# Optimization experiments

Measured on AMD Instinct MI355X. Metric: run time of the kernel, lower is better.

The kernel has to match this reference:

```python
import jax, jax.numpy as jnp
import numpy as np

ATTENTION_DIM = 256
MAX_STATE_SIZE = 2000
LOCATION_FILTER = 32
LOCATION_KERNEL = 31
TEMPERATURE = 1.0
CUMULATIVE = True
MASK_VAL = -2.0 ** 32 + 1


def setup_inputs() -> dict:
    key = jax.random.key(0)
    ks = jax.random.split(key, 8)
    B, T, A, F, K = 64, 2000, ATTENTION_DIM, LOCATION_FILTER, LOCATION_KERNEL
    query = jax.random.normal(ks[0], (B, A), dtype=jnp.float32)
    prev_weights = jax.random.uniform(ks[1], (B, MAX_STATE_SIZE), dtype=jnp.float32)
    w_memory = jax.random.normal(ks[2], (B, T, A), dtype=jnp.float32)
    memory_lengths = jax.random.randint(ks[3], (B,), 1, T + 1, dtype=jnp.int32)
    conv_w = jax.random.normal(ks[4], (K, 1, F), dtype=jnp.float32) * 0.1
    conv_b = jnp.zeros((F,), dtype=jnp.float32)
    loc_w = jax.random.normal(ks[5], (F, A), dtype=jnp.float32) * 0.1
    score_v = jax.random.normal(ks[6], (A,), dtype=jnp.float32)
    score_b = jnp.zeros((A,), dtype=jnp.float32)
    return {
        "query": query,
        "prev_weights": prev_weights,
        "w_memory": w_memory,
        "memory_lengths": memory_lengths,
        "conv_w": conv_w,
        "conv_b": conv_b,
        "loc_w": loc_w,
        "score_v": score_v,
        "score_b": score_b,
    }


def reference(query, prev_weights, w_memory, memory_lengths, conv_w, conv_b, loc_w, score_v, score_b):
    B, T, A = w_memory.shape
    # location features: conv over previous alignments [B, T, 1] -> [B, T, F]
    align_prev = prev_weights[:, :T][..., None]
    f = jax.lax.conv_general_dilated(
        align_prev, conv_w, window_strides=(1,), padding="SAME",
        dimension_numbers=("NWC", "WIO", "NWC")) + conv_b
    processed_loc = jnp.einsum("btf,fa->bta", f, loc_w)  # [B, T, A]
    # Bahdanau additive score -> [B, T]
    energy = jnp.einsum(
        "a,bta->bt", score_v,
        jnp.tanh(w_memory + query[:, None, :] + processed_loc + score_b)) / TEMPERATURE
    mask = jnp.arange(T)[None, :] < memory_lengths[:, None]
    energy = jnp.where(mask, energy, MASK_VAL)
    alignments = jax.nn.softmax(energy, axis=1)
    # pad to max_state_size (static pad amount)
    output = jnp.pad(alignments, ((0, 0), (0, MAX_STATE_SIZE - T)))
    new_weights = output + prev_weights if CUMULATIVE else output
    return output, new_weights
```

## Files before the change

### kernel.cpp

```cpp
#include <hip/hip_runtime.h>
#include <cstddef>

#define B_  64
#define T_  2000
#define A_  256
#define K_  31
#define F_  32
#define TT_ 128

__device__ __forceinline__ float fast_tanh(float x) {
  float p = __expf(x + x);
  float r = __builtin_amdgcn_rcpf(p + 1.0f);
  return fmaf(-2.0f, r, 1.0f);
}

__device__ __forceinline__ float4 ld4(const float* p) {
  return *(const float4*)p;
}

__device__ __forceinline__ float rfl(float x) {
  return __int_as_float(__builtin_amdgcn_readfirstlane(__float_as_int(x)));
}

__global__ __launch_bounds__(256) void prep_kernel(
    const float* __restrict__ conv_w, const float* __restrict__ conv_b,
    const float* __restrict__ loc_w, const float* __restrict__ query,
    const float* __restrict__ score_b, float* __restrict__ W2,
    float* __restrict__ qb) {
  const int a = threadIdx.x;
  const int blk = blockIdx.x;
  if (blk < K_) {
    float acc = 0.f;
    #pragma unroll
    for (int f = 0; f < F_; ++f) acc = fmaf(conv_w[blk * F_ + f], loc_w[f * A_ + a], acc);
    W2[blk * A_ + a] = acc;
  } else {
    const int b = blk - K_;
    float acc = 0.f;
    #pragma unroll
    for (int f = 0; f < F_; ++f) acc = fmaf(conv_b[f], loc_w[f * A_ + a], acc);
    qb[b * A_ + a] = query[b * A_ + a] + score_b[a] + acc;
  }
}

__global__ __attribute__((amdgpu_flat_work_group_size(256, 256),
                          amdgpu_waves_per_eu(2, 4)))
void energy_kernel(
    const float* __restrict__ wmem, const float* __restrict__ pw,
    const float* __restrict__ qb, const float* __restrict__ W2,
    const float* __restrict__ score_v, float* __restrict__ energy) {
  const int b = blockIdx.y;
  const int t0 = blockIdx.x * TT_;
  const int tid = threadIdx.x;
  const int lane = tid & 63;
  const int wv = tid >> 6;

  __shared__ __align__(16) float lds_W2[K_ * A_];
  __shared__ __align__(16) float lds_pw[TT_ + 36];

  for (int idx = tid * 4; idx < K_ * A_; idx += 256 * 4)
    *(float4*)&lds_W2[idx] = ld4(W2 + idx);

  if (tid < TT_ + 36) {
    const int g = t0 - 15 + tid;
    lds_pw[tid] = (g >= 0 && g < T_) ? pw[b * T_ + g] : 0.f;
  }
  __syncthreads();

  const float4 qb4 = ld4(qb + b * A_ + 4 * lane);
  const float4 v4  = ld4(score_v + 4 * lane);
  const float* wrow = wmem + (size_t)b * T_ * A_ + 4 * lane;
  const float* w2l  = lds_W2 + 4 * lane;

  const int rbase = 32 * wv;

  #pragma unroll 1
  for (int i = 0; i < 8; ++i) {
    const int widx = rbase + 4 * i;

    float4 w4[4];
    #pragma unroll
    for (int j = 0; j < 4; ++j) {
      const int t = t0 + widx + j;
      const int tc = t < T_ ? t : T_ - 1;
      w4[j] = ld4(wrow + (size_t)tc * A_);
    }

    float s[36];
    #pragma unroll
    for (int m = 0; m < 9; ++m) {
      const float4 t4 = ld4(&lds_pw[widx + 4 * m]);
      s[4 * m + 0] = rfl(t4.x); s[4 * m + 1] = rfl(t4.y);
      s[4 * m + 2] = rfl(t4.z); s[4 * m + 3] = rfl(t4.w);
    }

    float4 pl[4];
    #pragma unroll
    for (int j = 0; j < 4; ++j) pl[j] = make_float4(0.f, 0.f, 0.f, 0.f);
    #pragma unroll
    for (int k = 0; k < K_; ++k) {
      const float4 w2k = ld4(w2l + k * A_);
      #pragma unroll
      for (int j = 0; j < 4; ++j) {
        pl[j].x = fmaf(s[j + k], w2k.x, pl[j].x);
        pl[j].y = fmaf(s[j + k], w2k.y, pl[j].y);
        pl[j].z = fmaf(s[j + k], w2k.z, pl[j].z);
        pl[j].w = fmaf(s[j + k], w2k.w, pl[j].w);
      }
    }

    #pragma unroll
    for (int j = 0; j < 4; ++j) {
      const int t = t0 + widx + j;
      const float tx = fast_tanh(w4[j].x + qb4.x + pl[j].x);
      const float ty = fast_tanh(w4[j].y + qb4.y + pl[j].y);
      const float tz = fast_tanh(w4[j].z + qb4.z + pl[j].z);
      const float tw = fast_tanh(w4[j].w + qb4.w + pl[j].w);
      float e = fmaf(v4.x, tx, fmaf(v4.y, ty, fmaf(v4.z, tz, v4.w * tw)));
      #pragma unroll
      for (int m = 1; m < 64; m <<= 1) e += __shfl_xor(e, m, 64);
      if (lane == 0 && t < T_) energy[b * T_ + t] = e;
    }
  }
}

__global__ __launch_bounds__(256) void softmax_kernel(
    const float* __restrict__ energy, const float* __restrict__ pw,
    const int* __restrict__ lens, float* __restrict__ out) {
  const int b = blockIdx.x;
  const int tid = threadIdx.x;
  const int len = lens[b];
  __shared__ float red[4];
  const float L2E = 1.4426950408889634f;

  float mx = -3.4e38f;
  for (int t = tid; t < T_; t += 256)
    if (t < len) mx = fmaxf(mx, energy[b * T_ + t]);
  #pragma unroll
  for (int m = 1; m < 64; m <<= 1) mx = fmaxf(mx, __shfl_xor(mx, m, 64));
  if ((tid & 63) == 0) red[tid >> 6] = mx;
  __syncthreads();
  mx = fmaxf(fmaxf(red[0], red[1]), fmaxf(red[2], red[3]));
  __syncthreads();

  float sm = 0.f;
  for (int t = tid; t < T_; t += 256)
    if (t < len) sm += __builtin_amdgcn_exp2f((energy[b * T_ + t] - mx) * L2E);
  #pragma unroll
  for (int m = 1; m < 64; m <<= 1) sm += __shfl_xor(sm, m, 64);
  if ((tid & 63) == 0) red[tid >> 6] = sm;
  __syncthreads();
  sm = red[0] + red[1] + red[2] + red[3];
  const float inv = 1.0f / sm;

  for (int t = tid; t < T_; t += 256) {
    float o = 0.f;
    if (t < len)
      o = __builtin_amdgcn_exp2f((energy[b * T_ + t] - mx) * L2E) * inv;
    out[b * T_ + t] = o;
    out[B_ * T_ + b * T_ + t] = o + pw[b * T_ + t];
  }
}

extern "C" void kernel_launch(void* const* d_in, const int* in_sizes, int n_in,
                              void* d_out, int out_size, void* d_ws, size_t ws_size,
                              hipStream_t stream) {
  const float* query  = (const float*)d_in[0];
  const float* prev   = (const float*)d_in[1];
  const float* wmem   = (const float*)d_in[2];
  const int*   lens   = (const int*)d_in[3];
  const float* conv_w = (const float*)d_in[4];
  const float* conv_b = (const float*)d_in[5];
  const float* loc_w  = (const float*)d_in[6];
  const float* sv     = (const float*)d_in[7];
  const float* sb     = (const float*)d_in[8];
  float* out = (float*)d_out;
  float* ws  = (float*)d_ws;

  float* W2     = ws;
  float* qb     = ws + K_ * A_;
  float* energy = ws + K_ * A_ + B_ * A_;

  prep_kernel<<<K_ + B_, 256, 0, stream>>>(conv_w, conv_b, loc_w, query, sb, W2, qb);

  dim3 grid((T_ + TT_ - 1) / TT_, B_);
  energy_kernel<<<grid, 256, 0, stream>>>(wmem, prev, qb, W2, sv, energy);

  softmax_kernel<<<B_, 256, 0, stream>>>(energy, prev, lens, out);
}
```

Before: 233.0 us.

## Prefetch next w_memory rows and merge four row reductions into one butterfly

The energy loop now loads the next group of four w_memory rows while it computes the current group, using a software double buffer and a partial unroll of two. The four independent 64-lane wavefront reductions are replaced by a combined butterfly: two shuffle steps split the work between half-waves and quarter-waves, then a 16-lane reduction finishes all four rows at once. Four lanes then write the results. This aims to hide global-load latency and cut the shuffle count, at the cost of more live registers, which could lower occupancy.

```diff
diff --git a/kernel.cpp b/kernel.cpp
--- a/kernel.cpp
+++ b/kernel.cpp
@@ -74,16 +74,25 @@
 
   const int rbase = 32 * wv;
 
-  #pragma unroll 1
+  float4 w4[4], w4n[4];
+  #pragma unroll
+  for (int j = 0; j < 4; ++j) {
+    const int t = t0 + rbase + j;
+    const int tc = t < T_ ? t : T_ - 1;
+    w4[j] = ld4(wrow + (size_t)tc * A_);
+  }
+
+  #pragma unroll 2
   for (int i = 0; i < 8; ++i) {
     const int widx = rbase + 4 * i;
 
-    float4 w4[4];
-    #pragma unroll
-    for (int j = 0; j < 4; ++j) {
-      const int t = t0 + widx + j;
-      const int tc = t < T_ ? t : T_ - 1;
-      w4[j] = ld4(wrow + (size_t)tc * A_);
+    if (i < 7) {
+      #pragma unroll
+      for (int j = 0; j < 4; ++j) {
+        const int t = t0 + widx + 4 + j;
+        const int tc = t < T_ ? t : T_ - 1;
+        w4n[j] = ld4(wrow + (size_t)tc * A_);
+      }
     }
 
     float s[36];
@@ -109,18 +118,36 @@
       }
     }
 
+    float e[4];
     #pragma unroll
     for (int j = 0; j < 4; ++j) {
-      const int t = t0 + widx + j;
       const float tx = fast_tanh(w4[j].x + qb4.x + pl[j].x);
       const float ty = fast_tanh(w4[j].y + qb4.y + pl[j].y);
       const float tz = fast_tanh(w4[j].z + qb4.z + pl[j].z);
       const float tw = fast_tanh(w4[j].w + qb4.w + pl[j].w);
-      float e = fmaf(v4.x, tx, fmaf(v4.y, ty, fmaf(v4.z, tz, v4.w * tw)));
-      #pragma unroll
-      for (int m = 1; m < 64; m <<= 1) e += __shfl_xor(e, m, 64);
-      if (lane == 0 && t < T_) energy[b * T_ + t] = e;
-    }
+      e[j] = fmaf(v4.x, tx, fmaf(v4.y, ty, fmaf(v4.z, tz, v4.w * tw)));
+    }
+
+    #pragma unroll
+    for (int j = 0; j < 4; ++j) w4[j] = w4n[j];
+
+    float m0 = e[0] + __shfl_xor(e[0], 32);
+    float m1 = e[1] + __shfl_xor(e[1], 32);
+    float m2 = e[2] + __shfl_xor(e[2], 32);
+    float m3 = e[3] + __shfl_xor(e[3], 32);
+    const bool hi32 = (lane & 32) != 0;
+    float n0 = hi32 ? m2 : m0;
+    float n1 = hi32 ? m3 : m1;
+    float q0 = n0 + __shfl_xor(n0, 16);
+    float q1 = n1 + __shfl_xor(n1, 16);
+    float p = (lane & 16) ? q1 : q0;
+    p += __shfl_xor(p, 8);
+    p += __shfl_xor(p, 4);
+    p += __shfl_xor(p, 2);
+    p += __shfl_xor(p, 1);
+
+    const int tr = t0 + widx + (lane >> 4);
+    if ((lane & 15) == 0 && tr < T_) energy[b * T_ + tr] = p;
   }
 }
 
```

New measurement: 223.0 us. -4.3%, faster.

## Process eight rows per wave with packed FMAs and a transposed butterfly reduction

Applied to the files above, without the earlier changes.

The energy kernel now handles eight time rows per loop iteration instead of four, so each LDS weight load is reused across more rows. The location-conv accumulation uses two-wide vector FMAs, which can map to packed fp32 FMA instructions and roughly halve the VALU instruction count. The per-row 64-lane shuffle reductions are replaced by a transposed butterfly that reduces all eight rows together with far fewer cross-lane ops; lanes at multiples of 8 then write the results. The cost is higher register use for accumulators and the wider pw window, which could lower occupancy.

```diff
diff --git a/kernel.cpp b/kernel.cpp
--- a/kernel.cpp
+++ b/kernel.cpp
@@ -7,6 +7,9 @@
 #define K_  31
 #define F_  32
 #define TT_ 128
+#define RW_ 8
+
+typedef float v2f __attribute__((ext_vector_type(2)));
 
 __device__ __forceinline__ float fast_tanh(float x) {
   float p = __expf(x + x);
@@ -56,12 +59,12 @@
   const int wv = tid >> 6;
 
   __shared__ __align__(16) float lds_W2[K_ * A_];
-  __shared__ __align__(16) float lds_pw[TT_ + 36];
+  __shared__ __align__(16) float lds_pw[TT_ + 40];
 
   for (int idx = tid * 4; idx < K_ * A_; idx += 256 * 4)
     *(float4*)&lds_W2[idx] = ld4(W2 + idx);
 
-  if (tid < TT_ + 36) {
+  if (tid < TT_ + 40) {
     const int g = t0 - 15 + tid;
     lds_pw[tid] = (g >= 0 && g < T_) ? pw[b * T_ + g] : 0.f;
   }
@@ -75,52 +78,80 @@
   const int rbase = 32 * wv;
 
   #pragma unroll 1
-  for (int i = 0; i < 8; ++i) {
-    const int widx = rbase + 4 * i;
-
-    float4 w4[4];
-    #pragma unroll
-    for (int j = 0; j < 4; ++j) {
+  for (int i = 0; i < 32 / RW_; ++i) {
+    const int widx = rbase + RW_ * i;
+
+    float4 w4[RW_];
+    #pragma unroll
+    for (int j = 0; j < RW_; ++j) {
       const int t = t0 + widx + j;
       const int tc = t < T_ ? t : T_ - 1;
       w4[j] = ld4(wrow + (size_t)tc * A_);
     }
 
-    float s[36];
-    #pragma unroll
-    for (int m = 0; m < 9; ++m) {
+    float s[40];
+    #pragma unroll
+    for (int m = 0; m < 10; ++m) {
       const float4 t4 = ld4(&lds_pw[widx + 4 * m]);
       s[4 * m + 0] = rfl(t4.x); s[4 * m + 1] = rfl(t4.y);
       s[4 * m + 2] = rfl(t4.z); s[4 * m + 3] = rfl(t4.w);
     }
 
-    float4 pl[4];
-    #pragma unroll
-    for (int j = 0; j < 4; ++j) pl[j] = make_float4(0.f, 0.f, 0.f, 0.f);
+    v2f pl0[RW_], pl1[RW_];
+    #pragma unroll
+    for (int j = 0; j < RW_; ++j) { pl0[j] = (v2f)0.f; pl1[j] = (v2f)0.f; }
     #pragma unroll
     for (int k = 0; k < K_; ++k) {
       const float4 w2k = ld4(w2l + k * A_);
+      const v2f wa = {w2k.x, w2k.y};
+      const v2f wb = {w2k.z, w2k.w};
       #pragma unroll
-      for (int j = 0; j < 4; ++j) {
-        pl[j].x = fmaf(s[j + k], w2k.x, pl[j].x);
-        pl[j].y = fmaf(s[j + k], w2k.y, pl[j].y);
-        pl[j].z = fmaf(s[j + k], w2k.z, pl[j].z);
-        pl[j].w = fmaf(s[j + k], w2k.w, pl[j].w);
+      for (int j = 0; j < RW_; ++j) {
+        const v2f sv = {s[j + k], s[j + k]};
+        pl0[j] = __builtin_elementwise_fma(sv, wa, pl0[j]);
+        pl1[j] = __builtin_elementwise_fma(sv, wb, pl1[j]);
       }
     }
 
-    #pragma unroll
-    for (int j = 0; j < 4; ++j) {
-      const int t = t0 + widx + j;
-      const float tx = fast_tanh(w4[j].x + qb4.x + pl[j].x);
-      const float ty = fast_tanh(w4[j].y + qb4.y + pl[j].y);
-      const float tz = fast_tanh(w4[j].z + qb4.z + pl[j].z);
-      const float tw = fast_tanh(w4[j].w + qb4.w + pl[j].w);
-      float e = fmaf(v4.x, tx, fmaf(v4.y, ty, fmaf(v4.z, tz, v4.w * tw)));
-      #pragma unroll
-      for (int m = 1; m < 64; m <<= 1) e += __shfl_xor(e, m, 64);
-      if (lane == 0 && t < T_) energy[b * T_ + t] = e;
-    }
+    float e[RW_];
+    #pragma unroll
+    for (int j = 0; j < RW_; ++j) {
+      const float tx = fast_tanh(w4[j].x + qb4.x + pl0[j].x);
+      const float ty = fast_tanh(w4[j].y + qb4.y + pl0[j].y);
+      const float tz = fast_tanh(w4[j].z + qb4.z + pl1[j].x);
+      const float tw = fast_tanh(w4[j].w + qb4.w + pl1[j].y);
+      e[j] = fmaf(v4.x, tx, fmaf(v4.y, ty, fmaf(v4.z, tz, v4.w * tw)));
+    }
+
+    float m0 = e[0] + __shfl_xor(e[0], 32);
+    float m1 = e[1] + __shfl_xor(e[1], 32);
+    float m2 = e[2] + __shfl_xor(e[2], 32);
+    float m3 = e[3] + __shfl_xor(e[3], 32);
+    float m4 = e[4] + __shfl_xor(e[4], 32);
+    float m5 = e[5] + __shfl_xor(e[5], 32);
+    float m6 = e[6] + __shfl_xor(e[6], 32);
+    float m7 = e[7] + __shfl_xor(e[7], 32);
+    const bool b5 = (lane & 32) != 0;
+    float u0 = b5 ? m4 : m0;
+    float u1 = b5 ? m5 : m1;
+    float u2 = b5 ? m6 : m2;
+    float u3 = b5 ? m7 : m3;
+    u0 += __shfl_xor(u0, 16);
+    u1 += __shfl_xor(u1, 16);
+    u2 += __shfl_xor(u2, 16);
+    u3 += __shfl_xor(u3, 16);
+    const bool b4 = (lane & 16) != 0;
+    float w0 = b4 ? u2 : u0;
+    float w1 = b4 ? u3 : u1;
+    w0 += __shfl_xor(w0, 8);
+    w1 += __shfl_xor(w1, 8);
+    float y = (lane & 8) ? w1 : w0;
+    y += __shfl_xor(y, 4);
+    y += __shfl_xor(y, 2);
+    y += __shfl_xor(y, 1);
+
+    const int tr = t0 + widx + (lane >> 3);
+    if ((lane & 7) == 0 && tr < T_) energy[b * T_ + tr] = y;
   }
 }
 
```

Measured after the change: 224.5 us. 1.04x faster.
